# Kernel tuning notes

Measured on AMD Instinct MI355X. Metric: run time of the kernel, lower is better.

The kernel has to match this reference:

```python
import jax, jax.numpy as jnp
import numpy as np

N, M, D = 8192, 8192, 64

def setup_inputs() -> dict:
    key = jax.random.key(0)
    kx, ky = jax.random.split(key)
    x = jax.random.normal(kx, (N, D), dtype=jnp.float32)
    y = jax.random.normal(ky, (M, D), dtype=jnp.float32)
    sigma = jnp.array(1.0, dtype=jnp.float32)
    return {"x": x, "y": y, "sigma": sigma}

def reference(x, y, sigma):
    # Flatten trailing dims (no-op here since inputs are already 2-D).
    x2 = x.reshape(x.shape[0], -1)
    y2 = y.reshape(y.shape[0], -1)
    # Pairwise squared distances via the GEMM trick:
    # |x_i - y_j|^2 = |x_i|^2 + |y_j|^2 - 2 x_i . y_j
    xn = jnp.sum(x2 * x2, axis=1)            # [N]
    yn = jnp.sum(y2 * y2, axis=1)            # [M]
    cross = x2 @ y2.T                         # [N, M]
    sqd = xn[:, None] + yn[None, :] - 2.0 * cross
    sqd = jnp.maximum(sqd, 0.0)               # clamp tiny negatives from fp error
    return jnp.exp(-0.5 * sqd / (sigma * sigma))  # [N, M]
```

## Files before the change

kernel.cpp:

```cpp
#include <hip/hip_runtime.h>
#include <hip/hip_bf16.h>
#include <math.h>

#define N 8192
#define M 8192
#define D 64

typedef __bf16 bf16x8 __attribute__((ext_vector_type(8)));
typedef float f32x4 __attribute__((ext_vector_type(4)));

__global__ __launch_bounds__(256) void prep_kernel(
    const float* __restrict__ x, const float* __restrict__ y,
    __bf16* __restrict__ xsh, __bf16* __restrict__ xsl, float* __restrict__ xn,
    __bf16* __restrict__ ysh, __bf16* __restrict__ ysl, float* __restrict__ yn)
{
    int t   = threadIdx.x;
    int row = blockIdx.x * 32 + (t >> 3);
    int c   = t & 7;

    const float* src;
    __bf16 *ph, *pl;
    float* nrm;
    int r;
    bool isx = row < N;
    if (isx) { src = x; ph = xsh; pl = xsl; nrm = xn; r = row; }
    else     { src = y; ph = ysh; pl = ysl; nrm = yn; r = row - N; }

    const float* p = src + (size_t)r * D + c * 8;
    f32x4 a = *reinterpret_cast<const f32x4*>(p);
    f32x4 b = *reinterpret_cast<const f32x4*>(p + 4);
    float v[8] = {a[0], a[1], a[2], a[3], b[0], b[1], b[2], b[3]};

    bf16x8 hv, lv;
    float s = 0.0f;
    #pragma unroll
    for (int i = 0; i < 8; ++i) {
        float vi = v[i];
        __bf16 hi = (__bf16)vi;
        float lof = vi - (float)hi;
        hv[i] = hi;
        lv[i] = (__bf16)lof;
        s += vi * vi;
    }
    s += __shfl_down(s, 4);
    s += __shfl_down(s, 2);
    s += __shfl_down(s, 1);

    int g = r >> 6, m = r & 63;
    int slot;
    if (isx) slot = ((m >> 4) * 2 + (c >> 2)) * 64 + (c & 3) * 16 + (m & 15);
    else     slot = ((m & 3)  * 2 + (c >> 2)) * 64 + (c & 3) * 16 + (m >> 2);
    size_t idx = (size_t)g * 4096 + (size_t)slot * 8;

    *reinterpret_cast<bf16x8*>(ph + idx) = hv;
    *reinterpret_cast<bf16x8*>(pl + idx) = lv;
    if (c == 0) nrm[r] = s;
}

__global__ __launch_bounds__(256, 4) void rbf_kernel(
    const __bf16* __restrict__ xsh, const __bf16* __restrict__ xsl,
    const float* __restrict__ xn,
    const __bf16* __restrict__ ysh, const __bf16* __restrict__ ysl,
    const float* __restrict__ yn,
    const float* __restrict__ sig, float* __restrict__ out)
{
    int tid  = threadIdx.x;
    int wave = tid >> 6;
    int lane = tid & 63;
    int quad = lane >> 4;
    int l16  = lane & 15;

    int i_base = blockIdx.y * 128 + (wave >> 1) * 64;
    int j_base = blockIdx.x * 128 + (wave & 1) * 64;

    float s = sig[0];
    const float log2e = 1.4426950408889634f;
    float c  = -0.5f / (s * s) * log2e;
    float c2 = -2.0f * c;

    const __bf16* pbh = ysh + (size_t)(j_base >> 6) * 4096 + lane * 8;
    const __bf16* pbl = ysl + (size_t)(j_base >> 6) * 4096 + lane * 8;
    bf16x8 Bh[4][2], Bl[4][2];
    #pragma unroll
    for (int t = 0; t < 4; ++t)
        #pragma unroll
        for (int k = 0; k < 2; ++k) {
            Bh[t][k] = *reinterpret_cast<const bf16x8*>(pbh + (t * 2 + k) * 512);
            Bl[t][k] = *reinterpret_cast<const bf16x8*>(pbl + (t * 2 + k) * 512);
        }
    f32x4 ynv = *reinterpret_cast<const f32x4*>(yn + j_base + 4 * l16);

    const __bf16* pah = xsh + (size_t)(i_base >> 6) * 4096 + lane * 8;
    const __bf16* pal = xsl + (size_t)(i_base >> 6) * 4096 + lane * 8;

    #pragma unroll
    for (int ti = 0; ti < 4; ++ti) {
        bf16x8 Ah[2], Al[2];
        #pragma unroll
        for (int k = 0; k < 2; ++k) {
            Ah[k] = *reinterpret_cast<const bf16x8*>(pah + (ti * 2 + k) * 512);
            Al[k] = *reinterpret_cast<const bf16x8*>(pal + (ti * 2 + k) * 512);
        }
        f32x4 xnv = *reinterpret_cast<const f32x4*>(xn + i_base + ti * 16 + quad * 4);

        f32x4 acc[4];
        #pragma unroll
        for (int t = 0; t < 4; ++t) acc[t] = (f32x4){0.f, 0.f, 0.f, 0.f};

        #pragma unroll
        for (int k = 0; k < 2; ++k)
            #pragma unroll
            for (int t = 0; t < 4; ++t) {
                acc[t] = __builtin_amdgcn_mfma_f32_16x16x32_bf16(Ah[k], Bh[t][k], acc[t], 0, 0, 0);
                acc[t] = __builtin_amdgcn_mfma_f32_16x16x32_bf16(Ah[k], Bl[t][k], acc[t], 0, 0, 0);
                acc[t] = __builtin_amdgcn_mfma_f32_16x16x32_bf16(Al[k], Bh[t][k], acc[t], 0, 0, 0);
            }

        #pragma unroll
        for (int r = 0; r < 4; ++r) {
            int row = i_base + ti * 16 + quad * 4 + r;
            f32x4 v;
            #pragma unroll
            for (int t = 0; t < 4; ++t) {
                float arg = __builtin_fmaf(c2, acc[t][r], c * (xnv[r] + ynv[t]));
                arg = fminf(arg, 0.0f);
                v[t] = __builtin_amdgcn_exp2f(arg);
            }
            *reinterpret_cast<f32x4*>(out + (size_t)row * M + j_base + 4 * l16) = v;
        }
    }
}

extern "C" void kernel_launch(void* const* d_in, const int* in_sizes, int n_in,
                              void* d_out, int out_size, void* d_ws, size_t ws_size,
                              hipStream_t stream) {
    const float* x   = (const float*)d_in[0];
    const float* y   = (const float*)d_in[1];
    const float* sig = (const float*)d_in[2];
    float* out = (float*)d_out;

    char* ws = (char*)d_ws;
    __bf16* xsh = (__bf16*)(ws);
    __bf16* xsl = (__bf16*)(ws + (1u << 20));
    __bf16* ysh = (__bf16*)(ws + (2u << 20));
    __bf16* ysl = (__bf16*)(ws + (3u << 20));
    float*  xn  = (float*) (ws + (4u << 20));
    float*  yn  = (float*) (ws + (4u << 20) + (1u << 15));

    prep_kernel<<<(N + M) / 32, 256, 0, stream>>>(x, y, xsh, xsl, xn, ysh, ysl, yn);

    dim3 grid(M / 128, N / 128);
    rbf_kernel<<<grid, 256, 0, stream>>>(xsh, xsl, xn, ysh, ysl, yn, sig, out);
}
```

Measured before the change: 270.4 us.

## Loop each block over eight column tiles with register-prefetched B fragments

Each block now covers 1024 output columns instead of 128, iterating over eight 64-column tiles per wave while loading the next tile's B fragments and norms into registers ahead of use. The grid shrinks eightfold and the launch bound drops to two blocks per SIMD to allow more registers. The intent is to amortize per-block setup and hide global load latency of B under MFMA and exp work, at the cost of fewer resident waves and higher register pressure.

```diff
diff --git a/kernel.cpp b/kernel.cpp
--- a/kernel.cpp
+++ b/kernel.cpp
@@ -57,7 +57,7 @@
     if (c == 0) nrm[r] = s;
 }
 
-__global__ __launch_bounds__(256, 4) void rbf_kernel(
+__global__ __launch_bounds__(256, 2) void rbf_kernel(
     const __bf16* __restrict__ xsh, const __bf16* __restrict__ xsl,
     const float* __restrict__ xn,
     const __bf16* __restrict__ ysh, const __bf16* __restrict__ ysl,
@@ -71,62 +71,98 @@
     int l16  = lane & 15;
 
     int i_base = blockIdx.y * 128 + (wave >> 1) * 64;
-    int j_base = blockIdx.x * 128 + (wave & 1) * 64;
+    int j0     = blockIdx.x * 1024 + (wave & 1) * 512;
 
     float s = sig[0];
     const float log2e = 1.4426950408889634f;
     float c  = -0.5f / (s * s) * log2e;
     float c2 = -2.0f * c;
 
-    const __bf16* pbh = ysh + (size_t)(j_base >> 6) * 4096 + lane * 8;
-    const __bf16* pbl = ysl + (size_t)(j_base >> 6) * 4096 + lane * 8;
-    bf16x8 Bh[4][2], Bl[4][2];
+    const __bf16* pah = xsh + (size_t)(i_base >> 6) * 4096 + lane * 8;
+    const __bf16* pal = xsl + (size_t)(i_base >> 6) * 4096 + lane * 8;
+
+    f32x4 xnv[4];
+    #pragma unroll
+    for (int ti = 0; ti < 4; ++ti)
+        xnv[ti] = *reinterpret_cast<const f32x4*>(xn + i_base + ti * 16 + quad * 4);
+
+    const __bf16* pbh = ysh + (size_t)(j0 >> 6) * 4096 + lane * 8;
+    const __bf16* pbl = ysl + (size_t)(j0 >> 6) * 4096 + lane * 8;
+
+    bf16x8 BHc[4][2], BLc[4][2];
     #pragma unroll
     for (int t = 0; t < 4; ++t)
         #pragma unroll
         for (int k = 0; k < 2; ++k) {
-            Bh[t][k] = *reinterpret_cast<const bf16x8*>(pbh + (t * 2 + k) * 512);
-            Bl[t][k] = *reinterpret_cast<const bf16x8*>(pbl + (t * 2 + k) * 512);
+            BHc[t][k] = *reinterpret_cast<const bf16x8*>(pbh + (t * 2 + k) * 512);
+            BLc[t][k] = *reinterpret_cast<const bf16x8*>(pbl + (t * 2 + k) * 512);
         }
-    f32x4 ynv = *reinterpret_cast<const f32x4*>(yn + j_base + 4 * l16);
-
-    const __bf16* pah = xsh + (size_t)(i_base >> 6) * 4096 + lane * 8;
-    const __bf16* pal = xsl + (size_t)(i_base >> 6) * 4096 + lane * 8;
+    f32x4 ynv = *reinterpret_cast<const f32x4*>(yn + j0 + 4 * l16);
 
     #pragma unroll
-    for (int ti = 0; ti < 4; ++ti) {
-        bf16x8 Ah[2], Al[2];
-        #pragma unroll
-        for (int k = 0; k < 2; ++k) {
-            Ah[k] = *reinterpret_cast<const bf16x8*>(pah + (ti * 2 + k) * 512);
-            Al[k] = *reinterpret_cast<const bf16x8*>(pal + (ti * 2 + k) * 512);
+    for (int jt = 0; jt < 8; ++jt) {
+        int j = j0 + jt * 64;
+
+        bf16x8 BHn[4][2], BLn[4][2];
+        f32x4 ynvn;
+        if (jt < 7) {
+            const __bf16* nbh = pbh + (size_t)(jt + 1) * 4096;
+            const __bf16* nbl = pbl + (size_t)(jt + 1) * 4096;
+            #pragma unroll
+            for (int t = 0; t < 4; ++t)
+                #pragma unroll
+                for (int k = 0; k < 2; ++k) {
+                    BHn[t][k] = *reinterpret_cast<const bf16x8*>(nbh + (t * 2 + k) * 512);
+                    BLn[t][k] = *reinterpret_cast<const bf16x8*>(nbl + (t * 2 + k) * 512);
+                }
+            ynvn = *reinterpret_cast<const f32x4*>(yn + j + 64 + 4 * l16);
         }
-        f32x4 xnv = *reinterpret_cast<const f32x4*>(xn + i_base + ti * 16 + quad * 4);
-
-        f32x4 acc[4];
-        #pragma unroll
-        for (int t = 0; t < 4; ++t) acc[t] = (f32x4){0.f, 0.f, 0.f, 0.f};
 
         #pragma unroll
-        for (int k = 0; k < 2; ++k)
+        for (int ti = 0; ti < 4; ++ti) {
+            bf16x8 Ah[2], Al[2];
             #pragma unroll
-            for (int t = 0; t < 4; ++t) {
-                acc[t] = __builtin_amdgcn_mfma_f32_16x16x32_bf16(Ah[k], Bh[t][k], acc[t], 0, 0, 0);
-                acc[t] = __builtin_amdgcn_mfma_f32_16x16x32_bf16(Ah[k], Bl[t][k], acc[t], 0, 0, 0);
-                acc[t] = __builtin_amdgcn_mfma_f32_16x16x32_bf16(Al[k], Bh[t][k], acc[t], 0, 0, 0);
+            for (int k = 0; k < 2; ++k) {
+                Ah[k] = *reinterpret_cast<const bf16x8*>(pah + (ti * 2 + k) * 512);
+                Al[k] = *reinterpret_cast<const bf16x8*>(pal + (ti * 2 + k) * 512);
             }
 
-        #pragma unroll
-        for (int r = 0; r < 4; ++r) {
-            int row = i_base + ti * 16 + quad * 4 + r;
-            f32x4 v;
+            f32x4 acc[4];
             #pragma unroll
-            for (int t = 0; t < 4; ++t) {
-                float arg = __builtin_fmaf(c2, acc[t][r], c * (xnv[r] + ynv[t]));
-                arg = fminf(arg, 0.0f);
-                v[t] = __builtin_amdgcn_exp2f(arg);
+            for (int t = 0; t < 4; ++t) acc[t] = (f32x4){0.f, 0.f, 0.f, 0.f};
+
+            #pragma unroll
+            for (int k = 0; k < 2; ++k)
+                #pragma unroll
+                for (int t = 0; t < 4; ++t) {
+                    acc[t] = __builtin_amdgcn_mfma_f32_16x16x32_bf16(Ah[k], BHc[t][k], acc[t], 0, 0, 0);
+                    acc[t] = __builtin_amdgcn_mfma_f32_16x16x32_bf16(Ah[k], BLc[t][k], acc[t], 0, 0, 0);
+                    acc[t] = __builtin_amdgcn_mfma_f32_16x16x32_bf16(Al[k], BHc[t][k], acc[t], 0, 0, 0);
+                }
+
+            #pragma unroll
+            for (int r = 0; r < 4; ++r) {
+                int row = i_base + ti * 16 + quad * 4 + r;
+                f32x4 v;
+                #pragma unroll
+                for (int t = 0; t < 4; ++t) {
+                    float arg = __builtin_fmaf(c2, acc[t][r], c * (xnv[ti][r] + ynv[t]));
+                    arg = fminf(arg, 0.0f);
+                    v[t] = __builtin_amdgcn_exp2f(arg);
+                }
+                *reinterpret_cast<f32x4*>(out + (size_t)row * M + j + 4 * l16) = v;
             }
-            *reinterpret_cast<f32x4*>(out + (size_t)row * M + j_base + 4 * l16) = v;
+        }
+
+        if (jt < 7) {
+            #pragma unroll
+            for (int t = 0; t < 4; ++t)
+                #pragma unroll
+                for (int k = 0; k < 2; ++k) {
+                    BHc[t][k] = BHn[t][k];
+                    BLc[t][k] = BLn[t][k];
+                }
+            ynv = ynvn;
         }
     }
 }
@@ -149,6 +185,6 @@
 
     prep_kernel<<<(N + M) / 32, 256, 0, stream>>>(x, y, xsh, xsl, xn, ysh, ysl, yn);
 
-    dim3 grid(M / 128, N / 128);
+    dim3 grid(M / 1024, N / 128);
     rbf_kernel<<<grid, 256, 0, stream>>>(xsh, xsl, xn, ysh, ysl, yn, sig, out);
 }
```

New measurement: 271.4 us. Within noise of the previous version (+0.4%).
